# Optimization experiments

Hardware: AMD Instinct MI355X
Metric: run time of the kernel (lower is better)

The kernel has to match this reference:

```python
import jax, jax.numpy as jnp
import numpy as np

NUM_HEADS = 16
LN_EPS = 1e-5


def setup_inputs() -> dict:
    key = jax.random.key(0)
    ks = jax.random.split(key, 7)
    B, S, D = 4, 1024, 1024
    s_in = 1.0 / np.sqrt(D)
    return {
        "x": jax.random.normal(ks[0], (B, S, D), dtype=jnp.float32),
        # PyTorch MHA packed in-projection: [3D, D] weight, [3D] bias
        "w_qkv": jax.random.uniform(ks[1], (3 * D, D), dtype=jnp.float32, minval=-s_in, maxval=s_in),
        "b_qkv": jnp.zeros((3 * D,), dtype=jnp.float32),
        "w_out": jax.random.uniform(ks[2], (D, D), dtype=jnp.float32, minval=-s_in, maxval=s_in),
        "b_out": jnp.zeros((D,), dtype=jnp.float32),
        "ln_w": jnp.ones((D,), dtype=jnp.float32),
        "ln_b": jnp.zeros((D,), dtype=jnp.float32),
    }


def _layernorm(x, w, b):
    m = jnp.mean(x, axis=-1, keepdims=True)
    v = jnp.var(x, axis=-1, keepdims=True)
    return (x - m) * jax.lax.rsqrt(v + LN_EPS) * w + b


def reference(x, w_qkv, b_qkv, w_out, b_out, ln_w, ln_b):
    B, S, D = x.shape
    H = NUM_HEADS
    hd = D // H
    # packed QKV projection (torch: F.linear(x, w_qkv, b_qkv) then chunk)
    qkv = x @ w_qkv.T + b_qkv                      # [B, S, 3D]
    q, k, v = jnp.split(qkv, 3, axis=-1)
    q = q.reshape(B, S, H, hd).transpose(0, 2, 1, 3) * (hd ** -0.5)  # [B,H,S,hd]
    k = k.reshape(B, S, H, hd).transpose(0, 2, 1, 3)
    v = v.reshape(B, S, H, hd).transpose(0, 2, 1, 3)
    scores = jnp.einsum('bhqd,bhkd->bhqk', q, k)   # [B,H,S,S]
    attn = jax.nn.softmax(scores, axis=-1)
    ctx = jnp.einsum('bhqk,bhkd->bhqd', attn, v)   # [B,H,S,hd]
    ctx = ctx.transpose(0, 2, 1, 3).reshape(B, S, D)
    attn_out = ctx @ w_out.T + b_out
    # torch returns head-averaged weights (average_attn_weights=True)
    attn_weights = attn.mean(axis=1)               # [B,S,S]
    # dropout rate 0.0 -> identity; residual + LayerNorm
    y = _layernorm(x + attn_out, ln_w, ln_b)
    return y, attn_weights
```

## Files before the change

kernel.cpp:

```cpp
#include <hip/hip_runtime.h>
#include <cstdint>

typedef __bf16 bf16;
typedef __bf16 bf16x8 __attribute__((ext_vector_type(8)));
typedef __bf16 bf16x4 __attribute__((ext_vector_type(4)));
typedef float  f32x4  __attribute__((ext_vector_type(4)));

#define MFMA_BF16(a, b, c) __builtin_amdgcn_mfma_f32_16x16x32_bf16(a, b, c, 0, 0, 0)

__device__ __forceinline__ void async_load16(const void* g, void* l) {
    __builtin_amdgcn_global_load_lds(
        (__attribute__((address_space(1))) uint32_t*)(uintptr_t)g,
        (__attribute__((address_space(3))) uint32_t*)(uint32_t)(uintptr_t)l,
        16, 0, 0);
}

__global__ void cvt_kernel(const float* __restrict__ src, bf16* __restrict__ dst, int n4) {
    int i = blockIdx.x * blockDim.x + threadIdx.x;
    if (i < n4) {
        float4 v = ((const float4*)src)[i];
        bf16x4 o;
        o[0] = (bf16)v.x; o[1] = (bf16)v.y; o[2] = (bf16)v.z; o[3] = (bf16)v.w;
        ((bf16x4*)dst)[i] = o;
    }
}

__global__ __launch_bounds__(256) void gemm_qkv_kernel(
    const bf16* __restrict__ A, const bf16* __restrict__ W,
    const float* __restrict__ bias,
    bf16* __restrict__ Qb, bf16* __restrict__ Kb, bf16* __restrict__ Vt)
{
    const int Kd = 1024;
    __shared__ bf16 sA[128 * 32];
    __shared__ bf16 sB[128 * 32];
    int tid = threadIdx.x, lane = tid & 63, wid = tid >> 6;
    int m0 = blockIdx.y * 128, n0 = blockIdx.x * 128;
    int srow = wid * 32 + (lane >> 2);
    int scol = (lane & 3) * 8;
    const bf16* Ag = A + (size_t)(m0 + srow) * Kd + scol;
    const bf16* Wg = W + (size_t)(n0 + srow) * Kd + scol;
    bf16* sAp = &sA[srow * 32 + scol];
    bf16* sBp = &sB[srow * 32 + scol];
    int wm = (wid & 1) * 64, wn = (wid >> 1) * 64;
    int lcol = lane & 15, quad = lane >> 4;
    f32x4 acc[4][4] = {};
    for (int k0 = 0; k0 < Kd; k0 += 32) {
        __syncthreads();
        async_load16(Ag + k0, sAp);
        async_load16(Ag + k0 + 16 * Kd, sAp + 16 * 32);
        async_load16(Wg + k0, sBp);
        async_load16(Wg + k0 + 16 * Kd, sBp + 16 * 32);
        __syncthreads();
        bf16x8 af[4], bfr[4];
#pragma unroll
        for (int i = 0; i < 4; i++)
            af[i] = *(const bf16x8*)&sA[(wm + i * 16 + lcol) * 32 + quad * 8];
#pragma unroll
        for (int i = 0; i < 4; i++)
            bfr[i] = *(const bf16x8*)&sB[(wn + i * 16 + lcol) * 32 + quad * 8];
#pragma unroll
        for (int i = 0; i < 4; i++)
#pragma unroll
            for (int j = 0; j < 4; j++)
                acc[i][j] = MFMA_BF16(af[i], bfr[j], acc[i][j]);
    }
#pragma unroll
    for (int j = 0; j < 4; j++) {
        int n = n0 + wn + j * 16 + lcol;
        float bv = bias[n];
        int part = n >> 10, d = n & 1023, h = d >> 6, dd = d & 63;
#pragma unroll
        for (int i = 0; i < 4; i++) {
            int mb = m0 + wm + i * 16 + quad * 4;
            int b = mb >> 10, s = mb & 1023;
            if (part == 2) {
                bf16x4 v4;
#pragma unroll
                for (int r = 0; r < 4; r++) v4[r] = (bf16)(acc[i][j][r] + bv);
                *(bf16x4*)&Vt[(size_t)((b * 16 + h) * 64 + dd) * 1024 + s] = v4;
            } else {
                float scv = (part == 0) ? 0.125f : 1.0f;
                bf16* dst = (part == 0 ? Qb : Kb) + (size_t)((b * 16 + h) * 1024 + s) * 64 + dd;
#pragma unroll
                for (int r = 0; r < 4; r++) dst[(size_t)r * 64] = (bf16)((acc[i][j][r] + bv) * scv);
            }
        }
    }
}

__global__ __launch_bounds__(256) void gemm_out_kernel(
    const bf16* __restrict__ A, const bf16* __restrict__ W,
    const float* __restrict__ bias, float* __restrict__ out)
{
    const int Kd = 1024;
    __shared__ bf16 sA[2][128 * 32];
    __shared__ bf16 sB[2][128 * 32];
    int tid = threadIdx.x, lane = tid & 63, wid = tid >> 6;
    int m0 = blockIdx.y * 128, n0 = blockIdx.x * 128;
    int srow = wid * 32 + (lane >> 2);
    int scol = (lane & 3) * 8;
    const bf16* Ag = A + (size_t)(m0 + srow) * Kd + scol;
    const bf16* Wg = W + (size_t)(n0 + srow) * Kd + scol;
    int soff = srow * 32 + scol;
    int wm = (wid & 1) * 64, wn = (wid >> 1) * 64;
    int lcol = lane & 15, quad = lane >> 4;
    f32x4 acc[4][4] = {};
    async_load16(Ag, &sA[0][soff]);
    async_load16(Ag + 16 * Kd, &sA[0][soff + 512]);
    async_load16(Wg, &sB[0][soff]);
    async_load16(Wg + 16 * Kd, &sB[0][soff + 512]);
    int cur = 0;
    for (int k0 = 0; k0 < Kd; k0 += 32) {
        __syncthreads();
        if (k0 + 32 < Kd) {
            async_load16(Ag + k0 + 32, &sA[cur ^ 1][soff]);
            async_load16(Ag + k0 + 32 + 16 * Kd, &sA[cur ^ 1][soff + 512]);
            async_load16(Wg + k0 + 32, &sB[cur ^ 1][soff]);
            async_load16(Wg + k0 + 32 + 16 * Kd, &sB[cur ^ 1][soff + 512]);
        }
        bf16x8 af[4], bfr[4];
#pragma unroll
        for (int i = 0; i < 4; i++)
            af[i] = *(const bf16x8*)&sA[cur][(wm + i * 16 + lcol) * 32 + quad * 8];
#pragma unroll
        for (int i = 0; i < 4; i++)
            bfr[i] = *(const bf16x8*)&sB[cur][(wn + i * 16 + lcol) * 32 + quad * 8];
#pragma unroll
        for (int i = 0; i < 4; i++)
#pragma unroll
            for (int j = 0; j < 4; j++)
                acc[i][j] = MFMA_BF16(af[i], bfr[j], acc[i][j]);
        cur ^= 1;
    }
#pragma unroll
    for (int j = 0; j < 4; j++) {
        int n = n0 + wn + j * 16 + lcol;
        float bv = bias[n];
#pragma unroll
        for (int i = 0; i < 4; i++) {
            int m = m0 + wm + i * 16 + quad * 4;
#pragma unroll
            for (int r = 0; r < 4; r++) out[(size_t)(m + r) * 1024 + n] = acc[i][j][r] + bv;
        }
    }
}

__global__ __launch_bounds__(256) void flash_kernel(
    const bf16* __restrict__ Qb, const bf16* __restrict__ Kb, const bf16* __restrict__ Vt,
    bf16* __restrict__ ctx, float* __restrict__ ml)
{
    __shared__ bf16 sK[2][64 * 64];
    __shared__ bf16 sV[2][64 * 64];
    __shared__ bf16 pt[4][16 * 64];
    int tid = threadIdx.x, lane = tid & 63, wid = tid >> 6;
    int bx = blockIdx.x;
    int qt = bx & 15;
    int h = (bx >> 4) & 15;
    int b = bx >> 8;
    int lcol = lane & 15, quad = lane >> 4;
    size_t base = (size_t)(b * 16 + h) * 65536;

    int q0 = qt * 64 + wid * 16;
    const bf16* qp = Qb + base + (size_t)(q0 + lcol) * 64 + quad * 8;
    bf16x8 a0 = *(const bf16x8*)qp;
    bf16x8 a1 = *(const bf16x8*)(qp + 32);

    char* wpt = (char*)&pt[wid][0];
    int rr8 = lane >> 3;
    int pp  = lane & 7;
    int jj  = pp ^ rr8;
    int sr0 = wid * 16 + rr8;
    int sw  = lcol & 7;

#define STAGE_KV(buf, kt_) do { \
        async_load16(Kb + base + (size_t)((kt_) * 64 + sr0) * 64 + jj * 8,       &sK[buf][sr0 * 64 + pp * 8]); \
        async_load16(Kb + base + (size_t)((kt_) * 64 + sr0 + 8) * 64 + jj * 8,   &sK[buf][(sr0 + 8) * 64 + pp * 8]); \
        async_load16(Vt + base + (size_t)sr0 * 1024 + (kt_) * 64 + jj * 8,       &sV[buf][sr0 * 64 + pp * 8]); \
        async_load16(Vt + base + (size_t)(sr0 + 8) * 1024 + (kt_) * 64 + jj * 8, &sV[buf][(sr0 + 8) * 64 + pp * 8]); \
    } while (0)

    float l_[4] = {0.f, 0.f, 0.f, 0.f};
    f32x4 o[4] = {};

    STAGE_KV(0, 0);
    int cur = 0;
    for (int kt = 0; kt < 16; kt++) {
        __syncthreads();
        if (kt < 15) STAGE_KV(cur ^ 1, kt + 1);
        const bf16* sKc = &sK[cur][0];
        const bf16* sVc = &sV[cur][0];
#pragma unroll
        for (int nt = 0; nt < 4; nt++) {
            int ck = quad ^ sw;
            bf16x8 bk0 = *(const bf16x8*)&sKc[(nt * 16 + lcol) * 64 + ck * 8];
            bf16x8 bk1 = *(const bf16x8*)&sKc[(nt * 16 + lcol) * 64 + (ck ^ 4) * 8];
            f32x4 s = {};
            s = MFMA_BF16(a0, bk0, s);
            s = MFMA_BF16(a1, bk1, s);
#pragma unroll
            for (int rr = 0; rr < 4; rr++) {
                float p = __expf(s[rr]);
                l_[rr] += p;
                int row = quad * 4 + rr;
                *(bf16*)(wpt + row * 128 + ((nt * 32 + lcol * 2) ^ ((row & 7) << 4))) = (bf16)p;
            }
        }
#pragma unroll
        for (int kf = 0; kf < 2; kf++) {
            bf16x8 pa = *(const bf16x8*)(wpt + lcol * 128 + (((kf * 4 + quad) ^ sw) << 4));
#pragma unroll
            for (int dt = 0; dt < 4; dt++) {
                bf16x8 vb = *(const bf16x8*)&sVc[(dt * 16 + lcol) * 64 + ((kf * 4 + quad) ^ sw) * 8];
                o[dt] = MFMA_BF16(pa, vb, o[dt]);
            }
        }
        cur ^= 1;
    }
#undef STAGE_KV
#pragma unroll
    for (int mk = 1; mk < 16; mk <<= 1)
#pragma unroll
        for (int rr = 0; rr < 4; rr++) l_[rr] += __shfl_xor(l_[rr], mk, 64);
#pragma unroll
    for (int rr = 0; rr < 4; rr++) {
        float inv = 1.f / l_[rr];
        int qg = q0 + quad * 4 + rr;
#pragma unroll
        for (int dt = 0; dt < 4; dt++)
            ctx[(size_t)(b * 1024 + qg) * 1024 + h * 64 + dt * 16 + lcol] = (bf16)(o[dt][rr] * inv);
        if (lcol == 0)
            ml[(size_t)(b * 16 + h) * 1024 + qg] = l_[rr];
    }
}

__global__ __launch_bounds__(256) void aw_kernel(
    const bf16* __restrict__ Qb, const bf16* __restrict__ Kb,
    const float* __restrict__ ml, float* __restrict__ aw)
{
    __shared__ bf16 sK[2][64 * 64];
    int tid = threadIdx.x, lane = tid & 63, wid = tid >> 6;
    int bx = blockIdx.x;
    int kt = bx & 15;
    int qt = (bx >> 4) & 15;
    int b = bx >> 8;
    int lcol = lane & 15, quad = lane >> 4;
    int q0 = qt * 64 + wid * 16;
    int kbase = kt * 64;
    int sw = lcol & 7;
    int r0_ = tid >> 3, p0_ = tid & 7, j0_ = p0_ ^ (r0_ & 7);
    int r1_ = (tid + 256) >> 3, p1_ = (tid + 256) & 7, j1_ = p1_ ^ (r1_ & 7);

#define STAGE_K(buf, hh) do { \
        size_t hb_ = (size_t)(b * 16 + (hh)) * 65536; \
        async_load16(Kb + hb_ + (size_t)(kbase + r0_) * 64 + j0_ * 8, &sK[buf][(size_t)tid * 8]); \
        async_load16(Kb + hb_ + (size_t)(kbase + r1_) * 64 + j1_ * 8, &sK[buf][(size_t)(tid + 256) * 8]); \
    } while (0)

    float acc[16];
#pragma unroll
    for (int i = 0; i < 16; i++) acc[i] = 0.f;

    STAGE_K(0, 0);
    int cur = 0;
    for (int h = 0; h < 16; h++) {
        size_t base = (size_t)(b * 16 + h) * 65536;
        const bf16* qp = Qb + base + (size_t)(q0 + lcol) * 64 + quad * 8;
        bf16x8 a0 = *(const bf16x8*)qp;
        bf16x8 a1 = *(const bf16x8*)(qp + 32);
        float scale[4];
#pragma unroll
        for (int rr = 0; rr < 4; rr++)
            scale[rr] = 0.0625f / ml[(size_t)(b * 16 + h) * 1024 + q0 + quad * 4 + rr];
        __syncthreads();
        if (h < 15) STAGE_K(cur ^ 1, h + 1);
#pragma unroll
        for (int nt = 0; nt < 4; nt++) {
            int ck = quad ^ sw;
            bf16x8 bk0 = *(const bf16x8*)&sK[cur][(nt * 16 + lcol) * 64 + ck * 8];
            bf16x8 bk1 = *(const bf16x8*)&sK[cur][(nt * 16 + lcol) * 64 + (ck ^ 4) * 8];
            f32x4 s = {};
            s = MFMA_BF16(a0, bk0, s);
            s = MFMA_BF16(a1, bk1, s);
#pragma unroll
            for (int rr = 0; rr < 4; rr++)
                acc[nt * 4 + rr] += __expf(s[rr]) * scale[rr];
        }
        cur ^= 1;
    }
#undef STAGE_K
#pragma unroll
    for (int nt = 0; nt < 4; nt++)
#pragma unroll
        for (int rr = 0; rr < 4; rr++)
            aw[(size_t)(b * 1024 + q0 + quad * 4 + rr) * 1024 + kbase + nt * 16 + lcol] = acc[nt * 4 + rr];
}

__global__ __launch_bounds__(256) void ln_kernel(
    const float* __restrict__ x, const float* __restrict__ ao,
    const float* __restrict__ w, const float* __restrict__ bsh,
    float* __restrict__ y)
{
    int row = blockIdx.x, tid = threadIdx.x;
    float4 xv = ((const float4*)(x + (size_t)row * 1024))[tid];
    float4 av = ((const float4*)(ao + (size_t)row * 1024))[tid];
    float4 v = {xv.x + av.x, xv.y + av.y, xv.z + av.z, xv.w + av.w};
    float s = v.x + v.y + v.z + v.w;
    float ss = v.x * v.x + v.y * v.y + v.z * v.z + v.w * v.w;
#pragma unroll
    for (int off = 32; off; off >>= 1) { s += __shfl_down(s, off); ss += __shfl_down(ss, off); }
    __shared__ float rs[4], rss[4];
    int lane = tid & 63, wid = tid >> 6;
    if (lane == 0) { rs[wid] = s; rss[wid] = ss; }
    __syncthreads();
    s = rs[0] + rs[1] + rs[2] + rs[3];
    ss = rss[0] + rss[1] + rss[2] + rss[3];
    float mean = s * (1.f / 1024.f);
    float var = ss * (1.f / 1024.f) - mean * mean;
    float inv = rsqrtf(var + 1e-5f);
    float4 wv = ((const float4*)w)[tid];
    float4 bv = ((const float4*)bsh)[tid];
    float4 o;
    o.x = (v.x - mean) * inv * wv.x + bv.x;
    o.y = (v.y - mean) * inv * wv.y + bv.y;
    o.z = (v.z - mean) * inv * wv.z + bv.z;
    o.w = (v.w - mean) * inv * wv.w + bv.w;
    ((float4*)y)[row * 256 + tid] = o;
}

extern "C" void kernel_launch(void* const* d_in, const int* in_sizes, int n_in,
                              void* d_out, int out_size, void* d_ws, size_t ws_size,
                              hipStream_t stream) {
    const float* x     = (const float*)d_in[0];
    const float* w_qkv = (const float*)d_in[1];
    const float* b_qkv = (const float*)d_in[2];
    const float* w_out = (const float*)d_in[3];
    const float* b_out = (const float*)d_in[4];
    const float* ln_w  = (const float*)d_in[5];
    const float* ln_b  = (const float*)d_in[6];

    char* ws = (char*)d_ws;
    bf16*   Qb    = (bf16*)(ws);
    bf16*   Kb    = (bf16*)(ws + (8ull  << 20));
    bf16*   Vt    = (bf16*)(ws + (16ull << 20));
    bf16*   ctx   = (bf16*)(ws + (24ull << 20));
    float*  ml    = (float*)(ws + (32ull << 20));
    bf16*   x_bf  = (bf16*)(ws + (33ull << 20));
    bf16*   wq_bf = (bf16*)(ws + (41ull << 20));
    bf16*   wo_bf = (bf16*)(ws + (16ull << 20));
    float*  ao    = (float*)(ws);

    float* y_out  = (float*)d_out;
    float* aw_out = y_out + 4ull * 1024 * 1024;

    cvt_kernel<<<4096, 256, 0, stream>>>(x, x_bf, 1048576);
    cvt_kernel<<<3072, 256, 0, stream>>>(w_qkv, wq_bf, 786432);
    gemm_qkv_kernel<<<dim3(24, 32), 256, 0, stream>>>(x_bf, wq_bf, b_qkv, Qb, Kb, Vt);
    flash_kernel<<<1024, 256, 0, stream>>>(Qb, Kb, Vt, ctx, ml);
    aw_kernel<<<1024, 256, 0, stream>>>(Qb, Kb, ml, aw_out);
    cvt_kernel<<<1024, 256, 0, stream>>>(w_out, wo_bf, 262144);
    gemm_out_kernel<<<dim3(8, 32), 256, 0, stream>>>(ctx, wo_bf, b_out, ao);
    ln_kernel<<<4096, 256, 0, stream>>>(x, ao, ln_w, ln_b, y_out);
}
```

Measured before the change: 220.2 us.

## Double-buffer QKV GEMM with explicit waitcnt, halve out-GEMM tile, remap flash/aw blocks

The QKV projection GEMM switches from a single-buffered, fully synchronised loop to a two-stage prefetch pipeline that uses explicit vmcnt waits and raw barriers, so global-to-LDS loads overlap with MFMA work. The output GEMM gets the same pipeline and its M tile drops to 64, doubling the grid to 512 blocks for better CU occupancy. The flash and attention-weight kernels remap block indices so that consecutive blocks are spread across 8 groups, changing which blocks run concurrently (probably to spread them across XCDs for cache locality). The risks are reliance on hand-counted vmcnt values staying correct and a smaller output tile that gives less reuse per block.

```diff
diff --git a/kernel.cpp b/kernel.cpp
--- a/kernel.cpp
+++ b/kernel.cpp
@@ -7,6 +7,9 @@
 typedef float  f32x4  __attribute__((ext_vector_type(4)));
 
 #define MFMA_BF16(a, b, c) __builtin_amdgcn_mfma_f32_16x16x32_bf16(a, b, c, 0, 0, 0)
+
+#define WAITCNT_VM(n) asm volatile("s_waitcnt vmcnt(" #n ")" ::: "memory")
+#define CFENCE()      asm volatile("" ::: "memory")
 
 __device__ __forceinline__ void async_load16(const void* g, void* l) {
     __builtin_amdgcn_global_load_lds(
@@ -29,68 +32,6 @@
     const bf16* __restrict__ A, const bf16* __restrict__ W,
     const float* __restrict__ bias,
     bf16* __restrict__ Qb, bf16* __restrict__ Kb, bf16* __restrict__ Vt)
-{
-    const int Kd = 1024;
-    __shared__ bf16 sA[128 * 32];
-    __shared__ bf16 sB[128 * 32];
-    int tid = threadIdx.x, lane = tid & 63, wid = tid >> 6;
-    int m0 = blockIdx.y * 128, n0 = blockIdx.x * 128;
-    int srow = wid * 32 + (lane >> 2);
-    int scol = (lane & 3) * 8;
-    const bf16* Ag = A + (size_t)(m0 + srow) * Kd + scol;
-    const bf16* Wg = W + (size_t)(n0 + srow) * Kd + scol;
-    bf16* sAp = &sA[srow * 32 + scol];
-    bf16* sBp = &sB[srow * 32 + scol];
-    int wm = (wid & 1) * 64, wn = (wid >> 1) * 64;
-    int lcol = lane & 15, quad = lane >> 4;
-    f32x4 acc[4][4] = {};
-    for (int k0 = 0; k0 < Kd; k0 += 32) {
-        __syncthreads();
-        async_load16(Ag + k0, sAp);
-        async_load16(Ag + k0 + 16 * Kd, sAp + 16 * 32);
-        async_load16(Wg + k0, sBp);
-        async_load16(Wg + k0 + 16 * Kd, sBp + 16 * 32);
-        __syncthreads();
-        bf16x8 af[4], bfr[4];
-#pragma unroll
-        for (int i = 0; i < 4; i++)
-            af[i] = *(const bf16x8*)&sA[(wm + i * 16 + lcol) * 32 + quad * 8];
-#pragma unroll
-        for (int i = 0; i < 4; i++)
-            bfr[i] = *(const bf16x8*)&sB[(wn + i * 16 + lcol) * 32 + quad * 8];
-#pragma unroll
-        for (int i = 0; i < 4; i++)
-#pragma unroll
-            for (int j = 0; j < 4; j++)
-                acc[i][j] = MFMA_BF16(af[i], bfr[j], acc[i][j]);
-    }
-#pragma unroll
-    for (int j = 0; j < 4; j++) {
-        int n = n0 + wn + j * 16 + lcol;
-        float bv = bias[n];
-        int part = n >> 10, d = n & 1023, h = d >> 6, dd = d & 63;
-#pragma unroll
-        for (int i = 0; i < 4; i++) {
-            int mb = m0 + wm + i * 16 + quad * 4;
-            int b = mb >> 10, s = mb & 1023;
-            if (part == 2) {
-                bf16x4 v4;
-#pragma unroll
-                for (int r = 0; r < 4; r++) v4[r] = (bf16)(acc[i][j][r] + bv);
-                *(bf16x4*)&Vt[(size_t)((b * 16 + h) * 64 + dd) * 1024 + s] = v4;
-            } else {
-                float scv = (part == 0) ? 0.125f : 1.0f;
-                bf16* dst = (part == 0 ? Qb : Kb) + (size_t)((b * 16 + h) * 1024 + s) * 64 + dd;
-#pragma unroll
-                for (int r = 0; r < 4; r++) dst[(size_t)r * 64] = (bf16)((acc[i][j][r] + bv) * scv);
-            }
-        }
-    }
-}
-
-__global__ __launch_bounds__(256) void gemm_out_kernel(
-    const bf16* __restrict__ A, const bf16* __restrict__ W,
-    const float* __restrict__ bias, float* __restrict__ out)
 {
     const int Kd = 1024;
     __shared__ bf16 sA[2][128 * 32];
@@ -105,39 +46,114 @@
     int wm = (wid & 1) * 64, wn = (wid >> 1) * 64;
     int lcol = lane & 15, quad = lane >> 4;
     f32x4 acc[4][4] = {};
-    async_load16(Ag, &sA[0][soff]);
-    async_load16(Ag + 16 * Kd, &sA[0][soff + 512]);
-    async_load16(Wg, &sB[0][soff]);
-    async_load16(Wg + 16 * Kd, &sB[0][soff + 512]);
-    int cur = 0;
-    for (int k0 = 0; k0 < Kd; k0 += 32) {
-        __syncthreads();
-        if (k0 + 32 < Kd) {
-            async_load16(Ag + k0 + 32, &sA[cur ^ 1][soff]);
-            async_load16(Ag + k0 + 32 + 16 * Kd, &sA[cur ^ 1][soff + 512]);
-            async_load16(Wg + k0 + 32, &sB[cur ^ 1][soff]);
-            async_load16(Wg + k0 + 32 + 16 * Kd, &sB[cur ^ 1][soff + 512]);
-        }
+#define STG_Q(buf, k0_) do { \
+        async_load16(Ag + (k0_), &sA[buf][soff]); \
+        async_load16(Ag + (k0_) + 16 * Kd, &sA[buf][soff + 512]); \
+        async_load16(Wg + (k0_), &sB[buf][soff]); \
+        async_load16(Wg + (k0_) + 16 * Kd, &sB[buf][soff + 512]); \
+    } while (0)
+    STG_Q(0, 0);
+    STG_Q(1, 32);
+    for (int it = 0; it < 32; ++it) {
+        if (it < 31) { WAITCNT_VM(4); } else { WAITCNT_VM(0); }
+        __builtin_amdgcn_s_barrier();
+        CFENCE();
+        const bf16* cA = sA[it & 1];
+        const bf16* cB = sB[it & 1];
         bf16x8 af[4], bfr[4];
 #pragma unroll
         for (int i = 0; i < 4; i++)
-            af[i] = *(const bf16x8*)&sA[cur][(wm + i * 16 + lcol) * 32 + quad * 8];
+            af[i] = *(const bf16x8*)&cA[(wm + i * 16 + lcol) * 32 + quad * 8];
 #pragma unroll
         for (int i = 0; i < 4; i++)
-            bfr[i] = *(const bf16x8*)&sB[cur][(wn + i * 16 + lcol) * 32 + quad * 8];
+            bfr[i] = *(const bf16x8*)&cB[(wn + i * 16 + lcol) * 32 + quad * 8];
 #pragma unroll
         for (int i = 0; i < 4; i++)
 #pragma unroll
             for (int j = 0; j < 4; j++)
                 acc[i][j] = MFMA_BF16(af[i], bfr[j], acc[i][j]);
-        cur ^= 1;
-    }
+        CFENCE();
+        __builtin_amdgcn_s_barrier();
+        if (it + 2 < 32) STG_Q(it & 1, (it + 2) * 32);
+    }
+#undef STG_Q
 #pragma unroll
     for (int j = 0; j < 4; j++) {
         int n = n0 + wn + j * 16 + lcol;
         float bv = bias[n];
+        int part = n >> 10, d = n & 1023, h = d >> 6, dd = d & 63;
 #pragma unroll
         for (int i = 0; i < 4; i++) {
+            int mb = m0 + wm + i * 16 + quad * 4;
+            int b = mb >> 10, s = mb & 1023;
+            if (part == 2) {
+                bf16x4 v4;
+#pragma unroll
+                for (int r = 0; r < 4; r++) v4[r] = (bf16)(acc[i][j][r] + bv);
+                *(bf16x4*)&Vt[(size_t)((b * 16 + h) * 64 + dd) * 1024 + s] = v4;
+            } else {
+                float scv = (part == 0) ? 0.125f : 1.0f;
+                bf16* dst = (part == 0 ? Qb : Kb) + (size_t)((b * 16 + h) * 1024 + s) * 64 + dd;
+#pragma unroll
+                for (int r = 0; r < 4; r++) dst[(size_t)r * 64] = (bf16)((acc[i][j][r] + bv) * scv);
+            }
+        }
+    }
+}
+
+__global__ __launch_bounds__(256) void gemm_out_kernel(
+    const bf16* __restrict__ A, const bf16* __restrict__ W,
+    const float* __restrict__ bias, float* __restrict__ out)
+{
+    const int Kd = 1024;
+    __shared__ bf16 sA[2][64 * 32];
+    __shared__ bf16 sB[2][128 * 32];
+    int tid = threadIdx.x, lane = tid & 63, wid = tid >> 6;
+    int m0 = blockIdx.y * 64, n0 = blockIdx.x * 128;
+    int ra = tid >> 2;
+    int scol = (tid & 3) * 8;
+    const bf16* Ag = A + (size_t)(m0 + ra) * Kd + scol;
+    const bf16* Wg = W + (size_t)(n0 + ra) * Kd + scol;
+    int aoff = ra * 32 + scol;
+    int wm = (wid & 1) * 32, wn = (wid >> 1) * 64;
+    int lcol = lane & 15, quad = lane >> 4;
+    f32x4 acc[2][4] = {};
+#define STG_O(buf, k0_) do { \
+        async_load16(Ag + (k0_), &sA[buf][aoff]); \
+        async_load16(Wg + (k0_), &sB[buf][aoff]); \
+        async_load16(Wg + (k0_) + 64 * Kd, &sB[buf][aoff + 64 * 32]); \
+    } while (0)
+    STG_O(0, 0);
+    STG_O(1, 32);
+    for (int it = 0; it < 32; ++it) {
+        if (it < 31) { WAITCNT_VM(3); } else { WAITCNT_VM(0); }
+        __builtin_amdgcn_s_barrier();
+        CFENCE();
+        const bf16* cA = sA[it & 1];
+        const bf16* cB = sB[it & 1];
+        bf16x8 af[2], bfr[4];
+#pragma unroll
+        for (int i = 0; i < 2; i++)
+            af[i] = *(const bf16x8*)&cA[(wm + i * 16 + lcol) * 32 + quad * 8];
+#pragma unroll
+        for (int j = 0; j < 4; j++)
+            bfr[j] = *(const bf16x8*)&cB[(wn + j * 16 + lcol) * 32 + quad * 8];
+#pragma unroll
+        for (int i = 0; i < 2; i++)
+#pragma unroll
+            for (int j = 0; j < 4; j++)
+                acc[i][j] = MFMA_BF16(af[i], bfr[j], acc[i][j]);
+        CFENCE();
+        __builtin_amdgcn_s_barrier();
+        if (it + 2 < 32) STG_O(it & 1, (it + 2) * 32);
+    }
+#undef STG_O
+#pragma unroll
+    for (int j = 0; j < 4; j++) {
+        int n = n0 + wn + j * 16 + lcol;
+        float bv = bias[n];
+#pragma unroll
+        for (int i = 0; i < 2; i++) {
             int m = m0 + wm + i * 16 + quad * 4;
 #pragma unroll
             for (int r = 0; r < 4; r++) out[(size_t)(m + r) * 1024 + n] = acc[i][j][r] + bv;
@@ -154,9 +170,10 @@
     __shared__ bf16 pt[4][16 * 64];
     int tid = threadIdx.x, lane = tid & 63, wid = tid >> 6;
     int bx = blockIdx.x;
-    int qt = bx & 15;
-    int h = (bx >> 4) & 15;
-    int b = bx >> 8;
+    int orig = (bx & 7) * 128 + (bx >> 3);
+    int qt = orig & 15;
+    int h = (orig >> 4) & 15;
+    int b = orig >> 8;
     int lcol = lane & 15, quad = lane >> 4;
     size_t base = (size_t)(b * 16 + h) * 65536;
 
@@ -240,9 +257,10 @@
     __shared__ bf16 sK[2][64 * 64];
     int tid = threadIdx.x, lane = tid & 63, wid = tid >> 6;
     int bx = blockIdx.x;
-    int kt = bx & 15;
-    int qt = (bx >> 4) & 15;
-    int b = bx >> 8;
+    int orig = (bx & 7) * 128 + (bx >> 3);
+    int kt = orig & 15;
+    int qt = (orig >> 4) & 15;
+    int b = orig >> 8;
     int lcol = lane & 15, quad = lane >> 4;
     int q0 = qt * 64 + wid * 16;
     int kbase = kt * 64;
@@ -358,6 +376,6 @@
     flash_kernel<<<1024, 256, 0, stream>>>(Qb, Kb, Vt, ctx, ml);
     aw_kernel<<<1024, 256, 0, stream>>>(Qb, Kb, ml, aw_out);
     cvt_kernel<<<1024, 256, 0, stream>>>(w_out, wo_bf, 262144);
-    gemm_out_kernel<<<dim3(8, 32), 256, 0, stream>>>(ctx, wo_bf, b_out, ao);
+    gemm_out_kernel<<<dim3(8, 64), 256, 0, stream>>>(ctx, wo_bf, b_out, ao);
     ln_kernel<<<4096, 256, 0, stream>>>(x, ao, ln_w, ln_b, y_out);
 }
```

Result: no change. 221.4 us (+0.6%).
